# Optimization experiments

Hardware: AMD Instinct MI355X
Metric: run time of the kernel (lower is better)

## Reference

```python
import jax, jax.numpy as jnp
import numpy as np

B, DIM, NH, HD, H, W = 4, 64, 8, 8, 256, 256  # head_dim must equal num_heads (scale broadcast)


def setup_inputs() -> dict:
    key = jax.random.key(0)
    ks = jax.random.split(key, 10)
    s = 0.05
    return {
        "x": jax.random.normal(ks[0], (B, DIM, H, W), jnp.float32),
        "w3": jax.random.normal(ks[1], (DIM, 1, 3, 3), jnp.float32) * s,  # depthwise 3x3
        "b3": jax.random.normal(ks[2], (DIM,), jnp.float32) * s,
        "w5": jax.random.normal(ks[3], (DIM, 1, 5, 5), jnp.float32) * s,  # depthwise 5x5
        "b5": jax.random.normal(ks[4], (DIM,), jnp.float32) * s,
        "wqkv": jax.random.normal(ks[5], (3 * DIM, DIM), jnp.float32) * s,  # 1x1 conv, no bias
        "scale": jnp.ones((NH, 1, 1), jnp.float32),
        "g1_w": jax.random.normal(ks[6], (DIM // 4, DIM), jnp.float32) * s,
        "g1_b": jnp.zeros((DIM // 4,), jnp.float32),
        "g2_w": jax.random.normal(ks[7], (2, DIM // 4), jnp.float32) * s,
        "g2_b": jnp.zeros((2,), jnp.float32),
        "wp": jax.random.normal(ks[8], (DIM, DIM), jnp.float32) * s,  # 1x1 proj
        "bp": jnp.zeros((DIM,), jnp.float32),
    }


def _dwconv(x, w, b, pad):
    out = jax.lax.conv_general_dilated(
        x, w, (1, 1), [(pad, pad), (pad, pad)],
        dimension_numbers=("NCHW", "OIHW", "NCHW"), feature_group_count=x.shape[1])
    return out + b[None, :, None, None]


def _l2norm(t, eps=1e-12):  # F.normalize(dim=-1)
    n = jnp.sqrt(jnp.sum(t * t, axis=-1, keepdims=True))
    return t / jnp.maximum(n, eps)


def reference(x, w3, b3, w5, b5, wqkv, scale, g1_w, g1_b, g2_w, g2_b, wp, bp):
    b, c, h, w = x.shape
    conv_feat = _dwconv(x, w3, b3, 1) + _dwconv(x, w5, b5, 2)

    qkv = jnp.einsum("oc,bchw->bohw", wqkv, x)          # [b,3c,h,w]
    qkv = qkv.reshape(b, 3, NH, HD, h * w)
    q, k, v = qkv[:, 0], qkv[:, 1], qkv[:, 2]           # [b,NH,HD,hw]
    q = _l2norm(q)
    k = _l2norm(k)

    q_h = q.reshape(b, NH, HD, h, w)
    k_h = k.reshape(b, NH, HD, h, w)
    v_h = v.reshape(b, NH, HD, h, w)

    # row-axis attention: per (b,head,d-channel) attention over rows x (scale broadcasts onto HD axis)
    attn_h = jnp.einsum("bhdxy,bhdzy->bhdxz", q_h, k_h) * scale   # [b,NH,HD,h,h]
    attn_h = jax.nn.softmax(attn_h, axis=-1)
    out_h = jnp.einsum("bhdxz,bhdzy->bhdxy", attn_h, v_h).reshape(b, c, h, w)

    # column-axis attention (operate on transposed spatial layout)
    q_v = jnp.swapaxes(q_h, -1, -2)                      # [b,NH,HD,w,h]
    k_v = jnp.swapaxes(k_h, -1, -2)
    v_v = jnp.swapaxes(v_h, -1, -2)
    attn_v = jnp.einsum("bhdyx,bhdzx->bhdyz", q_v, k_v) * scale   # [b,NH,HD,w,w]
    attn_v = jax.nn.softmax(attn_v, axis=-1)
    out_v = jnp.einsum("bhdyz,bhdzx->bhdyx", attn_v, v_v)         # [b,NH,HD,w,h]
    out_v = jnp.swapaxes(out_v, -1, -2).reshape(b, c, h, w)

    attn_feat = out_h + out_v

    # global-pool gating: softmax over 2 mixing weights
    gx = jnp.mean(x, axis=(2, 3))                        # [b,c]
    h1 = jax.nn.relu(gx @ g1_w.T + g1_b)
    gw = jax.nn.softmax(h1 @ g2_w.T + g2_b, axis=1)      # [b,2]
    cw = gw[:, 0][:, None, None, None]
    aw = gw[:, 1][:, None, None, None]

    out = cw * conv_feat + aw * attn_feat
    return jnp.einsum("oc,bchw->bohw", wp, out) + bp[None, :, None, None]
```

## Files before the change

kernel.cpp:

```cpp
#include <hip/hip_runtime.h>
#include <stdint.h>


typedef unsigned short u16;
typedef __attribute__((ext_vector_type(8))) short bf16x8;
typedef __attribute__((ext_vector_type(4))) float f32x4;

#define DEV static __device__ __forceinline__

DEV u16 f2bf(float f) {
  unsigned u = __float_as_uint(f);
  return (u16)((u + 0x7fffu + ((u >> 16) & 1u)) >> 16);
}
DEV float bf2f(u16 h) { return __uint_as_float(((unsigned)h) << 16); }

__global__ void k_gx(const float* __restrict__ x, float* __restrict__ gxsum) {
  int bc = blockIdx.x, t = threadIdx.x;
  const float4* p = (const float4*)(x + ((size_t)bc << 16));
  float s = 0.f;
  for (int i = 0; i < 64; ++i) { float4 v = p[t + 256 * i]; s += v.x + v.y + v.z + v.w; }
  for (int off = 32; off; off >>= 1) s += __shfl_down(s, off);
  __shared__ float lds[4];
  if ((t & 63) == 0) lds[t >> 6] = s;
  __syncthreads();
  if (t == 0) gxsum[bc] = lds[0] + lds[1] + lds[2] + lds[3];
}

__global__ void k_gate(const float* __restrict__ gxsum, const float* __restrict__ g1w,
                       const float* __restrict__ g1b, const float* __restrict__ g2w,
                       const float* __restrict__ g2b, float* __restrict__ cwaw) {
  __shared__ float h1[4][16];
  int t = threadIdx.x;
  int b = t >> 4, j = t & 15;
  float a = g1b[j];
  for (int c = 0; c < 64; ++c) a += g1w[j * 64 + c] * gxsum[b * 64 + c] * (1.f / 65536.f);
  h1[b][j] = fmaxf(a, 0.f);
  __syncthreads();
  if (t < 4) {
    float l0 = g2b[0], l1 = g2b[1];
    for (int k = 0; k < 16; ++k) { l0 += g2w[k] * h1[t][k]; l1 += g2w[16 + k] * h1[t][k]; }
    float m = fmaxf(l0, l1);
    float e0 = __expf(l0 - m), e1 = __expf(l1 - m);
    float inv = 1.f / (e0 + e1);
    cwaw[t * 2 + 0] = e0 * inv;
    cwaw[t * 2 + 1] = e1 * inv;
  }
}

__global__ __launch_bounds__(256) void k_qkv(const float* __restrict__ x,
                                             const float* __restrict__ wqkv,
                                             u16* __restrict__ qkv) {
  __shared__ u16 Ws[192 * 72];
  __shared__ u16 Xs[128 * 72];
  int t = threadIdx.x;
  int b = blockIdx.x >> 9;
  int p0 = (blockIdx.x & 511) << 7;

  {
    int row = t >> 2, c0 = (t & 3) << 4;
#pragma unroll
    for (int i = 0; i < 3; ++i) {
      int r = i * 64 + row;
      const float* src = wqkv + r * 64 + c0;
      unsigned pk[8];
#pragma unroll
      for (int j = 0; j < 8; ++j)
        pk[j] = (unsigned)f2bf(src[2 * j]) | ((unsigned)f2bf(src[2 * j + 1]) << 16);
      uint4* dst = (uint4*)&Ws[r * 72 + c0];
      dst[0] = make_uint4(pk[0], pk[1], pk[2], pk[3]);
      dst[1] = make_uint4(pk[4], pk[5], pk[6], pk[7]);
    }
  }
  {
    int p = t & 127, ch = t >> 7;
    const float* xb = x + ((size_t)(b * 64) << 16) + p0 + p;
#pragma unroll
    for (int i = 0; i < 32; ++i) {
      int c = 2 * i + ch;
      Xs[p * 72 + c] = f2bf(xb[(size_t)c << 16]);
    }
  }
  __syncthreads();

  int w = t >> 6, l = t & 63, q = l >> 4, cl = l & 15;
  bf16x8 af[3][2];
#pragma unroll
  for (int g = 0; g < 3; ++g)
#pragma unroll
    for (int k = 0; k < 2; ++k)
      af[g][k] = *(const bf16x8*)&Ws[(w * 48 + g * 16 + cl) * 72 + k * 32 + q * 8];

  f32x4 acc[3][8];
  f32x4 zero = {0.f, 0.f, 0.f, 0.f};
#pragma unroll
  for (int g = 0; g < 3; ++g)
#pragma unroll
    for (int j = 0; j < 8; ++j) acc[g][j] = zero;

  for (int j = 0; j < 8; ++j) {
    bf16x8 b0 = *(const bf16x8*)&Xs[(j * 16 + cl) * 72 + q * 8];
    bf16x8 b1 = *(const bf16x8*)&Xs[(j * 16 + cl) * 72 + 32 + q * 8];
#pragma unroll
    for (int g = 0; g < 3; ++g) {
      acc[g][j] = __builtin_amdgcn_mfma_f32_16x16x32_bf16(af[g][0], b0, acc[g][j], 0, 0, 0);
      acc[g][j] = __builtin_amdgcn_mfma_f32_16x16x32_bf16(af[g][1], b1, acc[g][j], 0, 0, 0);
    }
  }
  u16* outb = qkv + ((size_t)(b * 192) << 16) + p0;
  for (int g = 0; g < 3; ++g) {
    int rowb = w * 48 + g * 16 + q * 4;
#pragma unroll
    for (int r = 0; r < 4; ++r) {
      u16* orow = outb + ((size_t)(rowb + r) << 16);
#pragma unroll
      for (int j = 0; j < 8; ++j) orow[j * 16 + cl] = f2bf(acc[g][j][r]);
    }
  }
}

__global__ void k_rnorm(const u16* __restrict__ qkv, float* __restrict__ rnorm) {
  int b = blockIdx.x >> 7, ch = blockIdx.x & 127;
  const uint2* p2 = (const uint2*)(qkv + ((size_t)(b * 192 + ch) << 16));
  int t = threadIdx.x;
  float s = 0.f;
  for (int i = 0; i < 64; ++i) {
    uint2 v = p2[t + 256 * i];
    float a = bf2f(v.x & 0xffff), bq = bf2f(v.x >> 16);
    float c = bf2f(v.y & 0xffff), d = bf2f(v.y >> 16);
    s += a * a + bq * bq + c * c + d * d;
  }
  for (int off = 32; off; off >>= 1) s += __shfl_down(s, off);
  __shared__ float lds[4];
  if ((t & 63) == 0) lds[t >> 6] = s;
  __syncthreads();
  if (t == 0) {
    float tot = lds[0] + lds[1] + lds[2] + lds[3];
    rnorm[blockIdx.x] = 1.f / fmaxf(sqrtf(tot), 1e-12f);
  }
}

__global__ __launch_bounds__(256) void k_tr(const u16* __restrict__ qkv,
                                            u16* __restrict__ qkvT) {
  int blk = blockIdx.x;
  int tile = blk & 15;
  int pl = blk >> 4;
  int b = pl >> 7, ch = pl & 127;
  int h0 = (tile >> 2) << 6, w0 = (tile & 3) << 6;
  const u16* ip = qkv + ((size_t)(b * 192 + ch) << 16);
  u16* op = qkvT + ((size_t)pl << 16);
  __shared__ unsigned lds32[64][33];
  int t = threadIdx.x;

  int r = t >> 2, qd = t & 3;
  uint4 v0 = *(const uint4*)&ip[(size_t)(h0 + r) * 256 + w0 + qd * 16];
  uint4 v1 = *(const uint4*)&ip[(size_t)(h0 + r) * 256 + w0 + qd * 16 + 8];
  unsigned vv[8] = {v0.x, v0.y, v0.z, v0.w, v1.x, v1.y, v1.z, v1.w};
#pragma unroll
  for (int k = 0; k < 8; ++k) lds32[r][qd * 8 + k] = vv[k];
  __syncthreads();

  int wl = t >> 2, hq = t & 3;
  unsigned pkout[8];
#pragma unroll
  for (int m = 0; m < 8; ++m) {
    unsigned a = lds32[hq * 16 + 2 * m][wl >> 1];
    unsigned b2 = lds32[hq * 16 + 2 * m + 1][wl >> 1];
    pkout[m] = (wl & 1) ? ((a >> 16) | (b2 & 0xffff0000u))
                        : ((a & 0xffffu) | (b2 << 16));
  }
  *(uint4*)&op[(size_t)(w0 + wl) * 256 + h0 + hq * 16] =
      make_uint4(pkout[0], pkout[1], pkout[2], pkout[3]);
  *(uint4*)&op[(size_t)(w0 + wl) * 256 + h0 + hq * 16 + 8] =
      make_uint4(pkout[4], pkout[5], pkout[6], pkout[7]);
}

__global__ void k_conv(const float* __restrict__ x, const float* __restrict__ w3,
                       const float* __restrict__ b3, const float* __restrict__ w5,
                       const float* __restrict__ b5, const float* __restrict__ cwaw,
                       float* __restrict__ outmix) {
  int rt = blockIdx.x & 31, bc = blockIdx.x >> 5, c = bc & 63, b = bc >> 6;
  int r0 = rt * 8;
  const float* xp = x + ((size_t)bc << 16);
  __shared__ float xs[12][256];
  int y = threadIdx.x;
  for (int rr = 0; rr < 12; ++rr) {
    int gr = r0 - 2 + rr;
    xs[rr][y] = (gr >= 0 && gr < 256) ? xp[(size_t)gr * 256 + y] : 0.f;
  }
  __syncthreads();
  float W3[9], W5[25];
#pragma unroll
  for (int i = 0; i < 9; ++i) W3[i] = w3[c * 9 + i];
#pragma unroll
  for (int i = 0; i < 25; ++i) W5[i] = w5[c * 25 + i];
  float bias = b3[c] + b5[c];
  float cw = cwaw[b * 2];
  float* op = outmix + ((size_t)bc << 16);
  for (int k = 0; k < 8; ++k) {
    float a = bias;
#pragma unroll
    for (int di = 0; di < 3; ++di)
#pragma unroll
      for (int dj = 0; dj < 3; ++dj) {
        int yy = y + dj - 1;
        float xv = (yy >= 0 && yy < 256) ? xs[k + 1 + di][yy] : 0.f;
        a += W3[di * 3 + dj] * xv;
      }
#pragma unroll
    for (int di = 0; di < 5; ++di)
#pragma unroll
      for (int dj = 0; dj < 5; ++dj) {
        int yy = y + dj - 2;
        float xv = (yy >= 0 && yy < 256) ? xs[k + di][yy] : 0.f;
        a += W5[di * 5 + dj] * xv;
      }
    op[(size_t)(r0 + k) * 256 + y] = cw * a;
  }
}

__global__ __launch_bounds__(256) void k_attn(
    const u16* __restrict__ qkv, const u16* __restrict__ qkvT,
    const float* __restrict__ rnorm, const float* __restrict__ scale,
    u16* __restrict__ oh, u16* __restrict__ ov) {
  __shared__ __align__(16) unsigned char smem[54272];
  u16* Pls = (u16*)smem;
  float* red = (float*)(smem + 33792);
  unsigned* Vt32 = (unsigned*)(smem + 33792);
  float* Osf = (float*)smem;

  int t = threadIdx.x;
  int w = t >> 6, l = t & 63, q = l >> 4, cl = l & 15;
  int idx = (blockIdx.x & 7) * 256 + (blockIdx.x >> 3);
  int rt = idx & 3, dir = (idx >> 2) & 1, c = (idx >> 3) & 63, b = idx >> 9;
  int r0 = rt << 6;

  const size_t P = 65536;
  const u16* Qp = dir ? qkvT + (size_t)(b * 128 + c) * P : qkv + (size_t)(b * 192 + c) * P;
  const u16* Kp = dir ? qkvT + (size_t)(b * 128 + 64 + c) * P : qkv + (size_t)(b * 192 + 64 + c) * P;
  const u16* Vp = qkv + (size_t)(b * 192 + 128 + c) * P;

  float sc = rnorm[b * 128 + c] * rnorm[b * 128 + 64 + c] * scale[c >> 3];

  f32x4 Sa[4][4];
  f32x4 zero = {0.f, 0.f, 0.f, 0.f};
#pragma unroll
  for (int i = 0; i < 4; ++i)
#pragma unroll
    for (int j = 0; j < 4; ++j) Sa[i][j] = zero;

  for (int yw = 0; yw < 8; ++yw) {
    int y0 = yw << 5;
    bf16x8 af[4], bfr[4];
#pragma unroll
    for (int i = 0; i < 4; ++i)
      af[i] = *(const bf16x8*)&Qp[(size_t)(r0 + i * 16 + cl) * 256 + y0 + q * 8];
#pragma unroll
    for (int j = 0; j < 4; ++j)
      bfr[j] = *(const bf16x8*)&Kp[(size_t)(w * 64 + j * 16 + cl) * 256 + y0 + q * 8];
#pragma unroll
    for (int i = 0; i < 4; ++i)
#pragma unroll
      for (int j = 0; j < 4; ++j)
        Sa[i][j] = __builtin_amdgcn_mfma_f32_16x16x32_bf16(af[i], bfr[j], Sa[i][j], 0, 0, 0);
  }

#pragma unroll
  for (int i = 0; i < 4; ++i)
#pragma unroll
    for (int j = 0; j < 4; ++j) Sa[i][j] *= sc;

  float mx[4][4], sm[4][4];
#pragma unroll
  for (int i = 0; i < 4; ++i)
#pragma unroll
    for (int r = 0; r < 4; ++r) {
      float m = fmaxf(fmaxf(Sa[i][0][r], Sa[i][1][r]), fmaxf(Sa[i][2][r], Sa[i][3][r]));
#pragma unroll
      for (int off = 1; off < 16; off <<= 1) m = fmaxf(m, __shfl_xor(m, off));
      mx[i][r] = m;
    }
  if (cl == 0) {
#pragma unroll
    for (int i = 0; i < 4; ++i)
#pragma unroll
      for (int r = 0; r < 4; ++r) red[w * 64 + i * 16 + q * 4 + r] = mx[i][r];
  }
  __syncthreads();
#pragma unroll
  for (int i = 0; i < 4; ++i)
#pragma unroll
    for (int r = 0; r < 4; ++r) {
      int rho = i * 16 + q * 4 + r;
      mx[i][r] = fmaxf(fmaxf(red[rho], red[64 + rho]), fmaxf(red[128 + rho], red[192 + rho]));
    }
  __syncthreads();
#pragma unroll
  for (int i = 0; i < 4; ++i)
#pragma unroll
    for (int r = 0; r < 4; ++r) {
      float s0 = 0.f;
#pragma unroll
      for (int j = 0; j < 4; ++j) {
        float e = __expf(Sa[i][j][r] - mx[i][r]);
        Sa[i][j][r] = e;
        s0 += e;
      }
#pragma unroll
      for (int off = 1; off < 16; off <<= 1) s0 += __shfl_xor(s0, off);
      sm[i][r] = s0;
    }
  if (cl == 0) {
#pragma unroll
    for (int i = 0; i < 4; ++i)
#pragma unroll
      for (int r = 0; r < 4; ++r) red[w * 64 + i * 16 + q * 4 + r] = sm[i][r];
  }
  __syncthreads();
#pragma unroll
  for (int i = 0; i < 4; ++i)
#pragma unroll
    for (int r = 0; r < 4; ++r) {
      int rho = i * 16 + q * 4 + r;
      sm[i][r] = 1.f / (red[rho] + red[64 + rho] + red[128 + rho] + red[192 + rho]);
    }
#pragma unroll
  for (int i = 0; i < 4; ++i)
#pragma unroll
    for (int r = 0; r < 4; ++r) {
      int rho = i * 16 + q * 4 + r;
#pragma unroll
      for (int j = 0; j < 4; ++j)
        Pls[rho * 264 + w * 64 + j * 16 + cl] = f2bf(Sa[i][j][r] * sm[i][r]);
    }
  __syncthreads();

  f32x4 Oa[4][4];
#pragma unroll
  for (int i = 0; i < 4; ++i)
#pragma unroll
    for (int j = 0; j < 4; ++j) Oa[i][j] = zero;

  if (dir == 0) {
    int z2 = t >> 4, colc = t & 15;
    int zlo = z2 & 3;
    int wkey = (((z2 >> 2) ^ (colc & 3)) << 2) + zlo;
    for (int zw = 0; zw < 8; ++zw) {
      int z0 = zw << 5;
      const u16* rp = Vp + (size_t)(z0 + 2 * z2) * 256 + colc * 16;
      uint4 a0 = *(const uint4*)rp;
      uint4 a1 = *(const uint4*)(rp + 8);
      uint4 c0 = *(const uint4*)(rp + 256);
      uint4 c1 = *(const uint4*)(rp + 264);
      unsigned A[8] = {a0.x, a0.y, a0.z, a0.w, a1.x, a1.y, a1.z, a1.w};
      unsigned Bv[8] = {c0.x, c0.y, c0.z, c0.w, c1.x, c1.y, c1.z, c1.w};
      __syncthreads();
#pragma unroll
      for (int m = 0; m < 16; ++m) {
        unsigned lo = (m & 1) ? (A[m >> 1] >> 16) : (A[m >> 1] & 0xffffu);
        unsigned hi = (m & 1) ? (Bv[m >> 1] & 0xffff0000u) : (Bv[m >> 1] << 16);
        Vt32[(colc * 16 + m) * 20 + wkey] = lo | hi;
      }
      __syncthreads();
      bf16x8 af[4], bfr[4];
#pragma unroll
      for (int i = 0; i < 4; ++i)
        af[i] = *(const bf16x8*)&Pls[(i * 16 + cl) * 264 + z0 + q * 8];
#pragma unroll
      for (int j = 0; j < 4; ++j) {
        int col = w * 64 + j * 16 + cl;
        bfr[j] = *(const bf16x8*)&Vt32[col * 20 + ((q ^ j) << 2)];
      }
#pragma unroll
      for (int i = 0; i < 4; ++i)
#pragma unroll
        for (int j = 0; j < 4; ++j)
          Oa[i][j] = __builtin_amdgcn_mfma_f32_16x16x32_bf16(af[i], bfr[j], Oa[i][j], 0, 0, 0);
    }
  } else {
    for (int zw = 0; zw < 8; ++zw) {
      int z0 = zw << 5;
      bf16x8 af[4], bfr[4];
#pragma unroll
      for (int i = 0; i < 4; ++i)
        af[i] = *(const bf16x8*)&Pls[(i * 16 + cl) * 264 + z0 + q * 8];
#pragma unroll
      for (int j = 0; j < 4; ++j)
        bfr[j] = *(const bf16x8*)&Vp[(size_t)(w * 64 + j * 16 + cl) * 256 + z0 + q * 8];
#pragma unroll
      for (int i = 0; i < 4; ++i)
#pragma unroll
        for (int j = 0; j < 4; ++j)
          Oa[i][j] = __builtin_amdgcn_mfma_f32_16x16x32_bf16(af[i], bfr[j], Oa[i][j], 0, 0, 0);
    }
  }

  if (dir == 0) {
    u16* op = oh + (size_t)(b * 64 + c) * P;
#pragma unroll
    for (int i = 0; i < 4; ++i)
#pragma unroll
      for (int j = 0; j < 4; ++j)
#pragma unroll
        for (int r = 0; r < 4; ++r)
          op[(size_t)(r0 + i * 16 + q * 4 + r) * 256 + w * 64 + j * 16 + cl] = f2bf(Oa[i][j][r]);
  } else {
    u16* op = ov + (size_t)(b * 64 + c) * P;
    __syncthreads();
    for (int h = 0; h < 2; ++h) {
#pragma unroll
      for (int ii = 0; ii < 2; ++ii) {
        int i = h * 2 + ii;
#pragma unroll
        for (int j = 0; j < 4; ++j)
#pragma unroll
          for (int r = 0; r < 4; ++r)
            Osf[(ii * 16 + q * 4 + r) * 260 + w * 64 + j * 16 + cl] = Oa[i][j][r];
      }
      __syncthreads();
      int rr = t & 31, xb = t >> 5;
      for (int xx = 0; xx < 32; ++xx) {
        int xcol = xx * 8 + xb;
        op[(size_t)xcol * 256 + r0 + h * 32 + rr] = f2bf(Osf[rr * 260 + xcol]);
      }
      __syncthreads();
    }
  }
}

__global__ __launch_bounds__(256) void k_final(
    float* __restrict__ dout, const u16* __restrict__ oh, const u16* __restrict__ ov,
    const float* __restrict__ wp, const float* __restrict__ bp,
    const float* __restrict__ cwaw) {
  __shared__ u16 Ms[256 * 72];
  __shared__ u16 Ws[64 * 72];
  int t = threadIdx.x;
  int b = blockIdx.x >> 8;
  int p0 = (blockIdx.x & 255) << 8;
  float aw = cwaw[b * 2 + 1];

  {
    int row = t >> 2, c0 = (t & 3) << 4;
    const float* src = wp + row * 64 + c0;
    unsigned pk[8];
#pragma unroll
    for (int j = 0; j < 8; ++j)
      pk[j] = (unsigned)f2bf(src[2 * j]) | ((unsigned)f2bf(src[2 * j + 1]) << 16);
    uint4* dst = (uint4*)&Ws[row * 72 + c0];
    dst[0] = make_uint4(pk[0], pk[1], pk[2], pk[3]);
    dst[1] = make_uint4(pk[4], pk[5], pk[6], pk[7]);
  }
  {
    size_t base = ((size_t)(b * 64) << 16) + p0 + t;
    for (int c = 0; c < 64; ++c) {
      size_t off = base + ((size_t)c << 16);
      float m = dout[off] + aw * (bf2f(oh[off]) + bf2f(ov[off]));
      Ms[t * 72 + c] = f2bf(m);
    }
  }
  __syncthreads();

  int w = t >> 6, l = t & 63, q = l >> 4, cl = l & 15;
  bf16x8 af0 = *(const bf16x8*)&Ws[(w * 16 + cl) * 72 + q * 8];
  bf16x8 af1 = *(const bf16x8*)&Ws[(w * 16 + cl) * 72 + 32 + q * 8];

  f32x4 acc[16];
  f32x4 zero = {0.f, 0.f, 0.f, 0.f};
#pragma unroll
  for (int j = 0; j < 16; ++j) acc[j] = zero;

  for (int j = 0; j < 16; ++j) {
    bf16x8 b0 = *(const bf16x8*)&Ms[(j * 16 + cl) * 72 + q * 8];
    bf16x8 b1 = *(const bf16x8*)&Ms[(j * 16 + cl) * 72 + 32 + q * 8];
    acc[j] = __builtin_amdgcn_mfma_f32_16x16x32_bf16(af0, b0, acc[j], 0, 0, 0);
    acc[j] = __builtin_amdgcn_mfma_f32_16x16x32_bf16(af1, b1, acc[j], 0, 0, 0);
  }

  float bpv[4];
#pragma unroll
  for (int r = 0; r < 4; ++r) bpv[r] = bp[w * 16 + q * 4 + r];
  float* outb = dout + ((size_t)(b * 64) << 16) + p0;
#pragma unroll
  for (int r = 0; r < 4; ++r) {
    float* orow = outb + ((size_t)(w * 16 + q * 4 + r) << 16);
#pragma unroll
    for (int j = 0; j < 16; ++j) orow[j * 16 + cl] = acc[j][r] + bpv[r];
  }
}

extern "C" void kernel_launch(void* const* d_in, const int* in_sizes, int n_in,
                              void* d_out, int out_size, void* d_ws, size_t ws_size,
                              hipStream_t stream) {
  const float* x = (const float*)d_in[0];
  const float* w3 = (const float*)d_in[1];
  const float* b3 = (const float*)d_in[2];
  const float* w5 = (const float*)d_in[3];
  const float* b5 = (const float*)d_in[4];
  const float* wqkv = (const float*)d_in[5];
  const float* scale = (const float*)d_in[6];
  const float* g1w = (const float*)d_in[7];
  const float* g1b = (const float*)d_in[8];
  const float* g2w = (const float*)d_in[9];
  const float* g2b = (const float*)d_in[10];
  const float* wp = (const float*)d_in[11];
  const float* bp = (const float*)d_in[12];
  float* out = (float*)d_out;

  char* ws = (char*)d_ws;
  u16* qkv = (u16*)(ws);
  u16* ohb = (u16*)(ws + 100663296ull);
  u16* ovb = (u16*)(ws + 134217728ull);
  float* fs = (float*)(ws + 167772160ull);
  float* gxsum = fs;
  float* cwaw = fs + 256;
  float* rnorm = fs + 264;
  u16* qkvT = (u16*)d_out;

  k_gx<<<256, 256, 0, stream>>>(x, gxsum);
  k_gate<<<1, 64, 0, stream>>>(gxsum, g1w, g1b, g2w, g2b, cwaw);
  k_qkv<<<2048, 256, 0, stream>>>(x, wqkv, qkv);
  k_rnorm<<<512, 256, 0, stream>>>(qkv, rnorm);
  k_tr<<<8192, 256, 0, stream>>>(qkv, qkvT);
  k_attn<<<2048, 256, 0, stream>>>(qkv, qkvT, rnorm, scale, ohb, ovb);
  k_conv<<<8192, 256, 0, stream>>>(x, w3, b3, w5, b5, cwaw, out);
  k_final<<<1024, 256, 0, stream>>>(out, ohb, ovb, wp, bp, cwaw);
}
```

Before: 391.3 us.

## Drop softmax max pass, swizzle P in LDS, split row-attention V transpose into halves

Removes the row-max reduction and its two barriers from the softmax, relying on q and k being L2-normalized so scaled logits stay bounded and exp without max subtraction is safe. The padded P buffer in LDS is replaced by an XOR-swizzled unpadded layout, shrinking shared memory from about 53 KB to 40 KB so more blocks can share a CU. For the row direction, the PV product is done in two column halves with a smaller V-transpose tile and half the accumulators, lowering register and LDS pressure at the cost of re-reading P from LDS twice. Skipping the max is only safe while the scale parameter stays small.

Result: slower. 420.0 us (+7.4%).

```diff
diff --git a/kernel.cpp b/kernel.cpp
--- a/kernel.cpp
+++ b/kernel.cpp
@@ -222,10 +222,10 @@
     const u16* __restrict__ qkv, const u16* __restrict__ qkvT,
     const float* __restrict__ rnorm, const float* __restrict__ scale,
     u16* __restrict__ oh, u16* __restrict__ ov) {
-  __shared__ __align__(16) unsigned char smem[54272];
+  __shared__ __align__(16) unsigned char smem[40960];
   u16* Pls = (u16*)smem;
-  float* red = (float*)(smem + 33792);
-  unsigned* Vt32 = (unsigned*)(smem + 33792);
+  float* red = (float*)(smem + 32768);
+  unsigned* Vt32 = (unsigned*)(smem + 32768);
   float* Osf = (float*)smem;
 
   int t = threadIdx.x;
@@ -264,36 +264,7 @@
         Sa[i][j] = __builtin_amdgcn_mfma_f32_16x16x32_bf16(af[i], bfr[j], Sa[i][j], 0, 0, 0);
   }
 
-#pragma unroll
-  for (int i = 0; i < 4; ++i)
-#pragma unroll
-    for (int j = 0; j < 4; ++j) Sa[i][j] *= sc;
-
-  float mx[4][4], sm[4][4];
-#pragma unroll
-  for (int i = 0; i < 4; ++i)
-#pragma unroll
-    for (int r = 0; r < 4; ++r) {
-      float m = fmaxf(fmaxf(Sa[i][0][r], Sa[i][1][r]), fmaxf(Sa[i][2][r], Sa[i][3][r]));
-#pragma unroll
-      for (int off = 1; off < 16; off <<= 1) m = fmaxf(m, __shfl_xor(m, off));
-      mx[i][r] = m;
-    }
-  if (cl == 0) {
-#pragma unroll
-    for (int i = 0; i < 4; ++i)
-#pragma unroll
-      for (int r = 0; r < 4; ++r) red[w * 64 + i * 16 + q * 4 + r] = mx[i][r];
-  }
-  __syncthreads();
-#pragma unroll
-  for (int i = 0; i < 4; ++i)
-#pragma unroll
-    for (int r = 0; r < 4; ++r) {
-      int rho = i * 16 + q * 4 + r;
-      mx[i][r] = fmaxf(fmaxf(red[rho], red[64 + rho]), fmaxf(red[128 + rho], red[192 + rho]));
-    }
-  __syncthreads();
+  float sm[4][4];
 #pragma unroll
   for (int i = 0; i < 4; ++i)
 #pragma unroll
@@ -301,7 +272,7 @@
       float s0 = 0.f;
 #pragma unroll
       for (int j = 0; j < 4; ++j) {
-        float e = __expf(Sa[i][j][r] - mx[i][r]);
+        float e = __expf(Sa[i][j][r] * sc);
         Sa[i][j][r] = e;
         s0 += e;
       }
@@ -328,61 +299,80 @@
 #pragma unroll
     for (int r = 0; r < 4; ++r) {
       int rho = i * 16 + q * 4 + r;
+      int sw = (rho & 7) << 3;
 #pragma unroll
       for (int j = 0; j < 4; ++j)
-        Pls[rho * 264 + w * 64 + j * 16 + cl] = f2bf(Sa[i][j][r] * sm[i][r]);
-    }
-  __syncthreads();
-
-  f32x4 Oa[4][4];
-#pragma unroll
-  for (int i = 0; i < 4; ++i)
-#pragma unroll
-    for (int j = 0; j < 4; ++j) Oa[i][j] = zero;
+        Pls[(rho * 256 + w * 64 + j * 16 + cl) ^ sw] = f2bf(Sa[i][j][r] * sm[i][r]);
+    }
+  __syncthreads();
 
   if (dir == 0) {
-    int z2 = t >> 4, colc = t & 15;
-    int zlo = z2 & 3;
-    int wkey = (((z2 >> 2) ^ (colc & 3)) << 2) + zlo;
-    for (int zw = 0; zw < 8; ++zw) {
-      int z0 = zw << 5;
-      const u16* rp = Vp + (size_t)(z0 + 2 * z2) * 256 + colc * 16;
-      uint4 a0 = *(const uint4*)rp;
-      uint4 a1 = *(const uint4*)(rp + 8);
-      uint4 c0 = *(const uint4*)(rp + 256);
-      uint4 c1 = *(const uint4*)(rp + 264);
-      unsigned A[8] = {a0.x, a0.y, a0.z, a0.w, a1.x, a1.y, a1.z, a1.w};
-      unsigned Bv[8] = {c0.x, c0.y, c0.z, c0.w, c1.x, c1.y, c1.z, c1.w};
-      __syncthreads();
-#pragma unroll
-      for (int m = 0; m < 16; ++m) {
-        unsigned lo = (m & 1) ? (A[m >> 1] >> 16) : (A[m >> 1] & 0xffffu);
-        unsigned hi = (m & 1) ? (Bv[m >> 1] & 0xffff0000u) : (Bv[m >> 1] << 16);
-        Vt32[(colc * 16 + m) * 20 + wkey] = lo | hi;
-      }
-      __syncthreads();
-      bf16x8 af[4], bfr[4];
+    int cc = t & 15, zp = t >> 4;
+    u16* opD = oh + (size_t)(b * 64 + c) * P;
+#pragma unroll
+    for (int p = 0; p < 2; ++p) {
+      f32x4 Oa2[4][2];
 #pragma unroll
       for (int i = 0; i < 4; ++i)
-        af[i] = *(const bf16x8*)&Pls[(i * 16 + cl) * 264 + z0 + q * 8];
-#pragma unroll
-      for (int j = 0; j < 4; ++j) {
-        int col = w * 64 + j * 16 + cl;
-        bfr[j] = *(const bf16x8*)&Vt32[col * 20 + ((q ^ j) << 2)];
+#pragma unroll
+        for (int jh = 0; jh < 2; ++jh) Oa2[i][jh] = zero;
+      for (int zw = 0; zw < 8; ++zw) {
+        int z0 = zw << 5;
+        const u16* rp = Vp + (size_t)(z0 + 2 * zp) * 256 + p * 128 + cc * 8;
+        uint4 a0 = *(const uint4*)rp;
+        uint4 a1 = *(const uint4*)(rp + 256);
+        unsigned A[4] = {a0.x, a0.y, a0.z, a0.w};
+        unsigned Bv[4] = {a1.x, a1.y, a1.z, a1.w};
+        __syncthreads();
+#pragma unroll
+        for (int m = 0; m < 8; ++m) {
+          unsigned lo = (A[m >> 1] >> ((m & 1) * 16)) & 0xffffu;
+          unsigned hi = (Bv[m >> 1] >> ((m & 1) * 16)) & 0xffffu;
+          int vcol = cc * 8 + m;
+          int g = (zp >> 2) ^ ((vcol >> 4) & 3);
+          Vt32[vcol * 16 + 4 * g + (zp & 3)] = lo | (hi << 16);
+        }
+        __syncthreads();
+        bf16x8 af[4], bfh[2];
+#pragma unroll
+        for (int i = 0; i < 4; ++i) {
+          int row = i * 16 + cl;
+          af[i] = *(const bf16x8*)&Pls[(row * 256 + z0 + q * 8) ^ ((row & 7) << 3)];
+        }
+#pragma unroll
+        for (int jh = 0; jh < 2; ++jh) {
+          int vcol = w * 32 + jh * 16 + cl;
+          bfh[jh] = *(const bf16x8*)&Vt32[vcol * 16 + 4 * (q ^ ((vcol >> 4) & 3))];
+        }
+#pragma unroll
+        for (int i = 0; i < 4; ++i)
+#pragma unroll
+          for (int jh = 0; jh < 2; ++jh)
+            Oa2[i][jh] = __builtin_amdgcn_mfma_f32_16x16x32_bf16(af[i], bfh[jh], Oa2[i][jh], 0, 0, 0);
       }
 #pragma unroll
       for (int i = 0; i < 4; ++i)
 #pragma unroll
-        for (int j = 0; j < 4; ++j)
-          Oa[i][j] = __builtin_amdgcn_mfma_f32_16x16x32_bf16(af[i], bfr[j], Oa[i][j], 0, 0, 0);
+        for (int jh = 0; jh < 2; ++jh)
+#pragma unroll
+          for (int r = 0; r < 4; ++r)
+            opD[(size_t)(r0 + i * 16 + q * 4 + r) * 256 + p * 128 + w * 32 + jh * 16 + cl] =
+                f2bf(Oa2[i][jh][r]);
     }
   } else {
+    f32x4 Oa[4][4];
+#pragma unroll
+    for (int i = 0; i < 4; ++i)
+#pragma unroll
+      for (int j = 0; j < 4; ++j) Oa[i][j] = zero;
     for (int zw = 0; zw < 8; ++zw) {
       int z0 = zw << 5;
       bf16x8 af[4], bfr[4];
 #pragma unroll
-      for (int i = 0; i < 4; ++i)
-        af[i] = *(const bf16x8*)&Pls[(i * 16 + cl) * 264 + z0 + q * 8];
+      for (int i = 0; i < 4; ++i) {
+        int row = i * 16 + cl;
+        af[i] = *(const bf16x8*)&Pls[(row * 256 + z0 + q * 8) ^ ((row & 7) << 3)];
+      }
 #pragma unroll
       for (int j = 0; j < 4; ++j)
         bfr[j] = *(const bf16x8*)&Vp[(size_t)(w * 64 + j * 16 + cl) * 256 + z0 + q * 8];
@@ -392,18 +382,6 @@
         for (int j = 0; j < 4; ++j)
           Oa[i][j] = __builtin_amdgcn_mfma_f32_16x16x32_bf16(af[i], bfr[j], Oa[i][j], 0, 0, 0);
     }
-  }
-
-  if (dir == 0) {
-    u16* op = oh + (size_t)(b * 64 + c) * P;
-#pragma unroll
-    for (int i = 0; i < 4; ++i)
-#pragma unroll
-      for (int j = 0; j < 4; ++j)
-#pragma unroll
-        for (int r = 0; r < 4; ++r)
-          op[(size_t)(r0 + i * 16 + q * 4 + r) * 256 + w * 64 + j * 16 + cl] = f2bf(Oa[i][j][r]);
-  } else {
     u16* op = ov + (size_t)(b * 64 + c) * P;
     __syncthreads();
     for (int h = 0; h < 2; ++h) {
```

## Halve attention row tile and drop softmax max-reduction pass

Applied to the files above, without the earlier changes.

Each attention block now handles 32 query rows instead of 64, and the grid doubles to 4096 blocks. This halves accumulator registers and cuts LDS to about 37 KB, with a launch-bounds hint aimed at more resident blocks per CU. Because q and k are L2-normalized, the row-max subtraction and its cross-wave reduction and barriers are removed, and exp is applied directly to the scaled scores. The trade-offs are that K and V are reloaded by twice as many blocks, and exp could overflow if the learned scale were very large.

After: 418.0 us. +6.8%, slower.

```diff
diff --git a/kernel.cpp b/kernel.cpp
--- a/kernel.cpp
+++ b/kernel.cpp
@@ -218,21 +218,21 @@
   }
 }
 
-__global__ __launch_bounds__(256) void k_attn(
+__global__ __launch_bounds__(256, 4) void k_attn(
     const u16* __restrict__ qkv, const u16* __restrict__ qkvT,
     const float* __restrict__ rnorm, const float* __restrict__ scale,
     u16* __restrict__ oh, u16* __restrict__ ov) {
-  __shared__ __align__(16) unsigned char smem[54272];
+  __shared__ __align__(16) unsigned char smem[37888];
   u16* Pls = (u16*)smem;
-  float* red = (float*)(smem + 33792);
-  unsigned* Vt32 = (unsigned*)(smem + 33792);
+  float* red = (float*)(smem + 16896);
+  unsigned* Vt32 = (unsigned*)(smem + 17408);
   float* Osf = (float*)smem;
 
   int t = threadIdx.x;
   int w = t >> 6, l = t & 63, q = l >> 4, cl = l & 15;
-  int idx = (blockIdx.x & 7) * 256 + (blockIdx.x >> 3);
-  int rt = idx & 3, dir = (idx >> 2) & 1, c = (idx >> 3) & 63, b = idx >> 9;
-  int r0 = rt << 6;
+  int idx = (blockIdx.x & 7) * 512 + (blockIdx.x >> 3);
+  int rt = idx & 7, dir = (idx >> 3) & 1, c = (idx >> 4) & 63, b = idx >> 10;
+  int r0 = rt << 5;
 
   const size_t P = 65536;
   const u16* Qp = dir ? qkvT + (size_t)(b * 128 + c) * P : qkv + (size_t)(b * 192 + c) * P;
@@ -241,67 +241,38 @@
 
   float sc = rnorm[b * 128 + c] * rnorm[b * 128 + 64 + c] * scale[c >> 3];
 
-  f32x4 Sa[4][4];
+  f32x4 Sa[2][4];
   f32x4 zero = {0.f, 0.f, 0.f, 0.f};
 #pragma unroll
-  for (int i = 0; i < 4; ++i)
+  for (int i = 0; i < 2; ++i)
 #pragma unroll
     for (int j = 0; j < 4; ++j) Sa[i][j] = zero;
 
   for (int yw = 0; yw < 8; ++yw) {
     int y0 = yw << 5;
-    bf16x8 af[4], bfr[4];
-#pragma unroll
-    for (int i = 0; i < 4; ++i)
+    bf16x8 af[2], bfr[4];
+#pragma unroll
+    for (int i = 0; i < 2; ++i)
       af[i] = *(const bf16x8*)&Qp[(size_t)(r0 + i * 16 + cl) * 256 + y0 + q * 8];
 #pragma unroll
     for (int j = 0; j < 4; ++j)
       bfr[j] = *(const bf16x8*)&Kp[(size_t)(w * 64 + j * 16 + cl) * 256 + y0 + q * 8];
 #pragma unroll
-    for (int i = 0; i < 4; ++i)
+    for (int i = 0; i < 2; ++i)
 #pragma unroll
       for (int j = 0; j < 4; ++j)
         Sa[i][j] = __builtin_amdgcn_mfma_f32_16x16x32_bf16(af[i], bfr[j], Sa[i][j], 0, 0, 0);
   }
 
-#pragma unroll
-  for (int i = 0; i < 4; ++i)
-#pragma unroll
-    for (int j = 0; j < 4; ++j) Sa[i][j] *= sc;
-
-  float mx[4][4], sm[4][4];
-#pragma unroll
-  for (int i = 0; i < 4; ++i)
-#pragma unroll
-    for (int r = 0; r < 4; ++r) {
-      float m = fmaxf(fmaxf(Sa[i][0][r], Sa[i][1][r]), fmaxf(Sa[i][2][r], Sa[i][3][r]));
-#pragma unroll
-      for (int off = 1; off < 16; off <<= 1) m = fmaxf(m, __shfl_xor(m, off));
-      mx[i][r] = m;
-    }
-  if (cl == 0) {
-#pragma unroll
-    for (int i = 0; i < 4; ++i)
-#pragma unroll
-      for (int r = 0; r < 4; ++r) red[w * 64 + i * 16 + q * 4 + r] = mx[i][r];
-  }
-  __syncthreads();
-#pragma unroll
-  for (int i = 0; i < 4; ++i)
-#pragma unroll
-    for (int r = 0; r < 4; ++r) {
-      int rho = i * 16 + q * 4 + r;
-      mx[i][r] = fmaxf(fmaxf(red[rho], red[64 + rho]), fmaxf(red[128 + rho], red[192 + rho]));
-    }
-  __syncthreads();
-#pragma unroll
-  for (int i = 0; i < 4; ++i)
+  float sm[2][4];
+#pragma unroll
+  for (int i = 0; i < 2; ++i)
 #pragma unroll
     for (int r = 0; r < 4; ++r) {
       float s0 = 0.f;
 #pragma unroll
       for (int j = 0; j < 4; ++j) {
-        float e = __expf(Sa[i][j][r] - mx[i][r]);
+        float e = __expf(Sa[i][j][r] * sc);
         Sa[i][j][r] = e;
         s0 += e;
       }
@@ -311,20 +282,20 @@
     }
   if (cl == 0) {
 #pragma unroll
-    for (int i = 0; i < 4; ++i)
-#pragma unroll
-      for (int r = 0; r < 4; ++r) red[w * 64 + i * 16 + q * 4 + r] = sm[i][r];
-  }
-  __syncthreads();
-#pragma unroll
-  for (int i = 0; i < 4; ++i)
+    for (int i = 0; i < 2; ++i)
+#pragma unroll
+      for (int r = 0; r < 4; ++r) red[w * 32 + i * 16 + q * 4 + r] = sm[i][r];
+  }
+  __syncthreads();
+#pragma unroll
+  for (int i = 0; i < 2; ++i)
 #pragma unroll
     for (int r = 0; r < 4; ++r) {
       int rho = i * 16 + q * 4 + r;
-      sm[i][r] = 1.f / (red[rho] + red[64 + rho] + red[128 + rho] + red[192 + rho]);
-    }
-#pragma unroll
-  for (int i = 0; i < 4; ++i)
+      sm[i][r] = 1.f / (red[rho] + red[32 + rho] + red[64 + rho] + red[96 + rho]);
+    }
+#pragma unroll
+  for (int i = 0; i < 2; ++i)
 #pragma unroll
     for (int r = 0; r < 4; ++r) {
       int rho = i * 16 + q * 4 + r;
@@ -334,9 +305,9 @@
     }
   __syncthreads();
 
-  f32x4 Oa[4][4];
-#pragma unroll
-  for (int i = 0; i < 4; ++i)
+  f32x4 Oa[2][4];
+#pragma unroll
+  for (int i = 0; i < 2; ++i)
 #pragma unroll
     for (int j = 0; j < 4; ++j) Oa[i][j] = zero;
 
@@ -361,9 +332,9 @@
         Vt32[(colc * 16 + m) * 20 + wkey] = lo | hi;
       }
       __syncthreads();
-      bf16x8 af[4], bfr[4];
-#pragma unroll
-      for (int i = 0; i < 4; ++i)
+      bf16x8 af[2], bfr[4];
+#pragma unroll
+      for (int i = 0; i < 2; ++i)
         af[i] = *(const bf16x8*)&Pls[(i * 16 + cl) * 264 + z0 + q * 8];
 #pragma unroll
       for (int j = 0; j < 4; ++j) {
@@ -371,58 +342,49 @@
         bfr[j] = *(const bf16x8*)&Vt32[col * 20 + ((q ^ j) << 2)];
       }
 #pragma unroll
-      for (int i = 0; i < 4; ++i)
+      for (int i = 0; i < 2; ++i)
 #pragma unroll
         for (int j = 0; j < 4; ++j)
           Oa[i][j] = __builtin_amdgcn_mfma_f32_16x16x32_bf16(af[i], bfr[j], Oa[i][j], 0, 0, 0);
     }
+    u16* op = oh + (size_t)(b * 64 + c) * P;
+#pragma unroll
+    for (int i = 0; i < 2; ++i)
+#pragma unroll
+      for (int j = 0; j < 4; ++j)
+#pragma unroll
+        for (int r = 0; r < 4; ++r)
+          op[(size_t)(r0 + i * 16 + q * 4 + r) * 256 + w * 64 + j * 16 + cl] = f2bf(Oa[i][j][r]);
   } else {
     for (int zw = 0; zw < 8; ++zw) {
       int z0 = zw << 5;
-      bf16x8 af[4], bfr[4];
-#pragma unroll
-      for (int i = 0; i < 4; ++i)
+      bf16x8 af[2], bfr[4];
+#pragma unroll
+      for (int i = 0; i < 2; ++i)
         af[i] = *(const bf16x8*)&Pls[(i * 16 + cl) * 264 + z0 + q * 8];
 #pragma unroll
       for (int j = 0; j < 4; ++j)
         bfr[j] = *(const bf16x8*)&Vp[(size_t)(w * 64 + j * 16 + cl) * 256 + z0 + q * 8];
 #pragma unroll
-      for (int i = 0; i < 4; ++i)
+      for (int i = 0; i < 2; ++i)
 #pragma unroll
         for (int j = 0; j < 4; ++j)
           Oa[i][j] = __builtin_amdgcn_mfma_f32_16x16x32_bf16(af[i], bfr[j], Oa[i][j], 0, 0, 0);
     }
-  }
-
-  if (dir == 0) {
-    u16* op = oh + (size_t)(b * 64 + c) * P;
-#pragma unroll
-    for (int i = 0; i < 4; ++i)
-#pragma unroll
-      for (int j = 0; j < 4; ++j)
-#pragma unroll
-        for (int r = 0; r < 4; ++r)
-          op[(size_t)(r0 + i * 16 + q * 4 + r) * 256 + w * 64 + j * 16 + cl] = f2bf(Oa[i][j][r]);
-  } else {
     u16* op = ov + (size_t)(b * 64 + c) * P;
     __syncthreads();
-    for (int h = 0; h < 2; ++h) {
-#pragma unroll
-      for (int ii = 0; ii < 2; ++ii) {
-        int i = h * 2 + ii;
-#pragma unroll
-        for (int j = 0; j < 4; ++j)
-#pragma unroll
-          for (int r = 0; r < 4; ++r)
-            Osf[(ii * 16 + q * 4 + r) * 260 + w * 64 + j * 16 + cl] = Oa[i][j][r];
-      }
-      __syncthreads();
-      int rr = t & 31, xb = t >> 5;
-      for (int xx = 0; xx < 32; ++xx) {
-        int xcol = xx * 8 + xb;
-        op[(size_t)xcol * 256 + r0 + h * 32 + rr] = f2bf(Osf[rr * 260 + xcol]);
-      }
-      __syncthreads();
+#pragma unroll
+    for (int i = 0; i < 2; ++i)
+#pragma unroll
+      for (int j = 0; j < 4; ++j)
+#pragma unroll
+        for (int r = 0; r < 4; ++r)
+          Osf[(i * 16 + q * 4 + r) * 260 + w * 64 + j * 16 + cl] = Oa[i][j][r];
+    __syncthreads();
+    int rr = t & 31, xb = t >> 5;
+    for (int xx = 0; xx < 32; ++xx) {
+      int xcol = xx * 8 + xb;
+      op[(size_t)xcol * 256 + r0 + rr] = f2bf(Osf[rr * 260 + xcol]);
     }
   }
 }
@@ -520,7 +482,7 @@
   k_qkv<<<2048, 256, 0, stream>>>(x, wqkv, qkv);
   k_rnorm<<<512, 256, 0, stream>>>(qkv, rnorm);
   k_tr<<<8192, 256, 0, stream>>>(qkv, qkvT);
-  k_attn<<<2048, 256, 0, stream>>>(qkv, qkvT, rnorm, scale, ohb, ovb);
+  k_attn<<<4096, 256, 0, stream>>>(qkv, qkvT, rnorm, scale, ohb, ovb);
   k_conv<<<8192, 256, 0, stream>>>(x, w3, b3, w5, b5, cwaw, out);
   k_final<<<1024, 256, 0, stream>>>(out, ohb, ovb, wp, bp, cwaw);
 }
```
